# Performance work log

Measured on AMD Instinct MI355X. Metric: run time of the kernel, lower is better.

## Reference

```python
import jax, jax.numpy as jnp
import numpy as np

N_SUBWORDS = 8192
N_WORDS = 6000
HIDDEN = 1024


def setup_inputs() -> dict:
    key = jax.random.key(0)
    k_h, k_s, k_w = jax.random.split(key, 3)
    hidden_states = jax.random.normal(k_h, (N_SUBWORDS, HIDDEN), dtype=jnp.float32)
    # sorted start indices of words; ends are inclusive and contiguous up to the next start
    word_starts = jnp.sort(jax.random.randint(k_s, (N_WORDS,), 0, N_SUBWORDS, dtype=jnp.int64))
    nxt = jnp.concatenate([word_starts[1:], jnp.array([N_SUBWORDS], dtype=jnp.int64)])
    word_ends = jnp.maximum(nxt - 1, word_starts)  # inclusive ends, >= starts
    # params of self.subword_attn = Linear(hidden_size, 1)
    w_attn = jax.random.normal(k_w, (HIDDEN, 1), dtype=jnp.float32) * 0.02
    b_attn = jnp.zeros((1,), dtype=jnp.float32)
    return {
        "hidden_states": hidden_states,
        "word_starts": word_starts,
        "word_ends": word_ends,
        "w_attn": w_attn,
        "b_attn": b_attn,
    }


def reference(hidden_states, word_starts, word_ends, w_attn, b_attn):
    """Word-encoder masked attention pooling (wl-coref _wordencoder_attn_scores + pooling).

    hidden_states: [n_subwords, hidden]
    word_starts/word_ends: [n_words] inclusive span boundaries over subwords
    Returns pooled word embeddings: [n_words, hidden]
    """
    n_sub = hidden_states.shape[0]
    pos = jnp.arange(n_sub)  # [n_subwords]
    # torch: (arange >= starts) * (arange < ends+1)  -> inclusive end mask
    mask = (pos[None, :] >= word_starts[:, None]) & (pos[None, :] <= word_ends[:, None])
    # per-subword scalar score: Linear(hidden, 1), broadcast to [n_words, n_subwords]
    scores = (hidden_states @ w_attn + b_attn).T  # [1, n_subwords]
    # torch adds log(mask.float()) == -inf outside span; scores are finite
    logits = jnp.where(mask, scores, -jnp.inf)
    attn = jax.nn.softmax(logits, axis=1)  # [n_words, n_subwords]
    # pool subword embeddings into word embeddings
    return attn @ hidden_states  # [n_words, hidden]
```

## Files before the change

### kernel.cpp

```cpp
#include <hip/hip_runtime.h>
#include <hip/hip_bf16.h>
#include <math.h>

#define N_SUBWORDS 8192
#define N_WORDS    6000
#define HIDDEN     1024

__global__ __launch_bounds__(256) void coref_fused_wave_kernel(
    const float* __restrict__ hs,
    const int*   __restrict__ starts,
    const int*   __restrict__ ends,
    const float* __restrict__ w_attn,
    const float* __restrict__ b_attn,
    float*       __restrict__ out)
{
    const int tid  = threadIdx.x;
    const int lane = tid & 63;
    const int w    = blockIdx.x * 4 + (tid >> 6);
    if (w >= N_WORDS) return;

    const int s0 = starts[w];
    const int s1 = ends[w];

    const float4* __restrict__ wvp = (const float4*)w_attn;
    float4 wv[4];
#pragma unroll
    for (int j = 0; j < 4; ++j)
        wv[j] = wvp[lane + 64 * j];
    const float b = b_attn[0];

    float  m = 0.f, l = 1.f;
    float4 acc[4];

    for (int s = s0; s <= s1; ++s) {
        const float4* __restrict__ row = (const float4*)(hs + (size_t)s * HIDDEN);
        float4 h[4];
#pragma unroll
        for (int j = 0; j < 4; ++j)
            h[j] = row[lane + 64 * j];

        float part = 0.f;
#pragma unroll
        for (int j = 0; j < 4; ++j)
            part += h[j].x * wv[j].x + h[j].y * wv[j].y +
                    h[j].z * wv[j].z + h[j].w * wv[j].w;

#pragma unroll
        for (int off = 32; off > 0; off >>= 1)
            part += __shfl_xor(part, off, 64);

        const float score = part + b;

        if (s == s0) {
            m = score;
            l = 1.f;
#pragma unroll
            for (int j = 0; j < 4; ++j)
                acc[j] = h[j];
        } else {
            const float mn    = fmaxf(m, score);
            const float alpha = __expf(m - mn);
            const float p     = __expf(score - mn);
            m = mn;
            l = l * alpha + p;
#pragma unroll
            for (int j = 0; j < 4; ++j) {
                acc[j].x = acc[j].x * alpha + p * h[j].x;
                acc[j].y = acc[j].y * alpha + p * h[j].y;
                acc[j].z = acc[j].z * alpha + p * h[j].z;
                acc[j].w = acc[j].w * alpha + p * h[j].w;
            }
        }
    }

    const float inv_l = 1.f / l;
    float4* __restrict__ orow = (float4*)(out + (size_t)w * HIDDEN);
#pragma unroll
    for (int j = 0; j < 4; ++j) {
        float4 o;
        o.x = acc[j].x * inv_l;
        o.y = acc[j].y * inv_l;
        o.z = acc[j].z * inv_l;
        o.w = acc[j].w * inv_l;
        orow[lane + 64 * j] = o;
    }
}

extern "C" void kernel_launch(void* const* d_in, const int* in_sizes, int n_in,
                              void* d_out, int out_size, void* d_ws, size_t ws_size,
                              hipStream_t stream) {
    const float* hs     = (const float*)d_in[0];
    const int*   starts = (const int*)d_in[1];
    const int*   ends   = (const int*)d_in[2];
    const float* w_attn = (const float*)d_in[3];
    const float* b_attn = (const float*)d_in[4];
    float*       out    = (float*)d_out;

    coref_fused_wave_kernel<<<dim3((N_WORDS + 3) / 4), dim3(256), 0, stream>>>(
        hs, starts, ends, w_attn, b_attn, out);
}
```

Before: 90.86 us.

## Split score computation into separate kernel and use two-pass softmax pooling

```diff
diff --git a/kernel.cpp b/kernel.cpp
--- a/kernel.cpp
+++ b/kernel.cpp
@@ -1,17 +1,45 @@
 #include <hip/hip_runtime.h>
-#include <hip/hip_bf16.h>
 #include <math.h>
 
 #define N_SUBWORDS 8192
 #define N_WORDS    6000
 #define HIDDEN     1024
 
-__global__ __launch_bounds__(256) void coref_fused_wave_kernel(
+__global__ __launch_bounds__(256) void coref_score_kernel(
+    const float* __restrict__ hs,
+    const float* __restrict__ w_attn,
+    const float* __restrict__ b_attn,
+    float*       __restrict__ scores)
+{
+    const int tid  = threadIdx.x;
+    const int lane = tid & 63;
+    const int row  = blockIdx.x * 4 + (tid >> 6);
+    if (row >= N_SUBWORDS) return;
+
+    const float4* __restrict__ wvp = (const float4*)w_attn;
+    const float4* __restrict__ rp  = (const float4*)(hs + (size_t)row * HIDDEN);
+
+    float part = 0.f;
+#pragma unroll
+    for (int j = 0; j < 4; ++j) {
+        const float4 h  = rp[lane + 64 * j];
+        const float4 wv = wvp[lane + 64 * j];
+        part += h.x * wv.x + h.y * wv.y + h.z * wv.z + h.w * wv.w;
+    }
+
+#pragma unroll
+    for (int off = 32; off > 0; off >>= 1)
+        part += __shfl_xor(part, off, 64);
+
+    if (lane == 0)
+        scores[row] = part + b_attn[0];
+}
+
+__global__ __launch_bounds__(256) void coref_pool_kernel(
     const float* __restrict__ hs,
     const int*   __restrict__ starts,
     const int*   __restrict__ ends,
-    const float* __restrict__ w_attn,
-    const float* __restrict__ b_attn,
+    const float* __restrict__ scores,
     float*       __restrict__ out)
 {
     const int tid  = threadIdx.x;
@@ -22,54 +50,27 @@
     const int s0 = starts[w];
     const int s1 = ends[w];
 
-    const float4* __restrict__ wvp = (const float4*)w_attn;
-    float4 wv[4];
+    float m = -INFINITY;
+    for (int s = s0; s <= s1; ++s)
+        m = fmaxf(m, scores[s]);
+
+    float  l = 0.f;
+    float4 acc[4];
 #pragma unroll
     for (int j = 0; j < 4; ++j)
-        wv[j] = wvp[lane + 64 * j];
-    const float b = b_attn[0];
-
-    float  m = 0.f, l = 1.f;
-    float4 acc[4];
+        acc[j] = make_float4(0.f, 0.f, 0.f, 0.f);
 
     for (int s = s0; s <= s1; ++s) {
+        const float p = __expf(scores[s] - m);
+        l += p;
         const float4* __restrict__ row = (const float4*)(hs + (size_t)s * HIDDEN);
-        float4 h[4];
 #pragma unroll
-        for (int j = 0; j < 4; ++j)
-            h[j] = row[lane + 64 * j];
-
-        float part = 0.f;
-#pragma unroll
-        for (int j = 0; j < 4; ++j)
-            part += h[j].x * wv[j].x + h[j].y * wv[j].y +
-                    h[j].z * wv[j].z + h[j].w * wv[j].w;
-
-#pragma unroll
-        for (int off = 32; off > 0; off >>= 1)
-            part += __shfl_xor(part, off, 64);
-
-        const float score = part + b;
-
-        if (s == s0) {
-            m = score;
-            l = 1.f;
-#pragma unroll
-            for (int j = 0; j < 4; ++j)
-                acc[j] = h[j];
-        } else {
-            const float mn    = fmaxf(m, score);
-            const float alpha = __expf(m - mn);
-            const float p     = __expf(score - mn);
-            m = mn;
-            l = l * alpha + p;
-#pragma unroll
-            for (int j = 0; j < 4; ++j) {
-                acc[j].x = acc[j].x * alpha + p * h[j].x;
-                acc[j].y = acc[j].y * alpha + p * h[j].y;
-                acc[j].z = acc[j].z * alpha + p * h[j].z;
-                acc[j].w = acc[j].w * alpha + p * h[j].w;
-            }
+        for (int j = 0; j < 4; ++j) {
+            const float4 h = row[lane + 64 * j];
+            acc[j].x += p * h.x;
+            acc[j].y += p * h.y;
+            acc[j].z += p * h.z;
+            acc[j].w += p * h.w;
         }
     }
 
@@ -95,7 +96,11 @@
     const float* w_attn = (const float*)d_in[3];
     const float* b_attn = (const float*)d_in[4];
     float*       out    = (float*)d_out;
+    float*       scores = (float*)d_ws;
 
-    coref_fused_wave_kernel<<<dim3((N_WORDS + 3) / 4), dim3(256), 0, stream>>>(
-        hs, starts, ends, w_attn, b_attn, out);
+    coref_score_kernel<<<dim3(N_SUBWORDS / 4), dim3(256), 0, stream>>>(
+        hs, w_attn, b_attn, scores);
+
+    coref_pool_kernel<<<dim3((N_WORDS + 3) / 4), dim3(256), 0, stream>>>(
+        hs, starts, ends, scores, out);
 }
```

Measured after the change: 96.32 us. 6.0% more time.

## Process four subword rows per online-softmax step and fast-path single-subword words

Applied to the files above, without the earlier changes.

```diff
diff --git a/kernel.cpp b/kernel.cpp
--- a/kernel.cpp
+++ b/kernel.cpp
@@ -1,12 +1,11 @@
 #include <hip/hip_runtime.h>
-#include <hip/hip_bf16.h>
 #include <math.h>
 
 #define N_SUBWORDS 8192
 #define N_WORDS    6000
 #define HIDDEN     1024
 
-__global__ __launch_bounds__(256) void coref_fused_wave_kernel(
+__global__ __launch_bounds__(256) void coref_fused_kernel(
     const float* __restrict__ hs,
     const int*   __restrict__ starts,
     const int*   __restrict__ ends,
@@ -16,11 +15,22 @@
 {
     const int tid  = threadIdx.x;
     const int lane = tid & 63;
-    const int w    = blockIdx.x * 4 + (tid >> 6);
+    const int w = __builtin_amdgcn_readfirstlane(blockIdx.x * 4 + (tid >> 6));
     if (w >= N_WORDS) return;
 
     const int s0 = starts[w];
     const int s1 = ends[w];
+
+    const float4* __restrict__ hs4  = (const float4*)hs;
+    float4*       __restrict__ orow = (float4*)(out + (size_t)w * HIDDEN);
+
+    if (s1 <= s0) {
+        const float4* __restrict__ row = hs4 + (size_t)s0 * (HIDDEN / 4);
+#pragma unroll
+        for (int j = 0; j < 4; ++j)
+            orow[lane + 64 * j] = row[lane + 64 * j];
+        return;
+    }
 
     const float4* __restrict__ wvp = (const float4*)w_attn;
     float4 wv[4];
@@ -29,52 +39,75 @@
         wv[j] = wvp[lane + 64 * j];
     const float b = b_attn[0];
 
-    float  m = 0.f, l = 1.f;
+    float  m = -INFINITY, l = 0.f;
     float4 acc[4];
+#pragma unroll
+    for (int j = 0; j < 4; ++j)
+        acc[j] = make_float4(0.f, 0.f, 0.f, 0.f);
 
-    for (int s = s0; s <= s1; ++s) {
-        const float4* __restrict__ row = (const float4*)(hs + (size_t)s * HIDDEN);
-        float4 h[4];
+    for (int s = s0; s <= s1; s += 4) {
+        const int C = (s1 - s + 1 < 4) ? (s1 - s + 1) : 4;
+
+        float4 h[4][4];
+        float  part[4];
 #pragma unroll
-        for (int j = 0; j < 4; ++j)
-            h[j] = row[lane + 64 * j];
-
-        float part = 0.f;
+        for (int c = 0; c < 4; ++c) {
+            part[c] = 0.f;
+            if (c < C) {
+                const float4* __restrict__ row =
+                    hs4 + (size_t)(s + c) * (HIDDEN / 4);
 #pragma unroll
-        for (int j = 0; j < 4; ++j)
-            part += h[j].x * wv[j].x + h[j].y * wv[j].y +
-                    h[j].z * wv[j].z + h[j].w * wv[j].w;
+                for (int j = 0; j < 4; ++j) {
+                    h[c][j] = row[lane + 64 * j];
+                    part[c] += h[c][j].x * wv[j].x + h[c][j].y * wv[j].y +
+                               h[c][j].z * wv[j].z + h[c][j].w * wv[j].w;
+                }
+            }
+        }
 
 #pragma unroll
-        for (int off = 32; off > 0; off >>= 1)
-            part += __shfl_xor(part, off, 64);
+        for (int off = 32; off > 0; off >>= 1) {
+#pragma unroll
+            for (int c = 0; c < 4; ++c)
+                part[c] += __shfl_xor(part[c], off, 64);
+        }
 
-        const float score = part + b;
+        float cm = -INFINITY;
+#pragma unroll
+        for (int c = 0; c < 4; ++c)
+            if (c < C) cm = fmaxf(cm, part[c] + b);
 
-        if (s == s0) {
-            m = score;
-            l = 1.f;
+        const float mn    = fmaxf(m, cm);
+        const float alpha = __expf(m - mn);
+        l *= alpha;
 #pragma unroll
-            for (int j = 0; j < 4; ++j)
-                acc[j] = h[j];
-        } else {
-            const float mn    = fmaxf(m, score);
-            const float alpha = __expf(m - mn);
-            const float p     = __expf(score - mn);
-            m = mn;
-            l = l * alpha + p;
+        for (int j = 0; j < 4; ++j) {
+            acc[j].x *= alpha; acc[j].y *= alpha;
+            acc[j].z *= alpha; acc[j].w *= alpha;
+        }
+
+        float p[4];
 #pragma unroll
-            for (int j = 0; j < 4; ++j) {
-                acc[j].x = acc[j].x * alpha + p * h[j].x;
-                acc[j].y = acc[j].y * alpha + p * h[j].y;
-                acc[j].z = acc[j].z * alpha + p * h[j].z;
-                acc[j].w = acc[j].w * alpha + p * h[j].w;
+        for (int c = 0; c < 4; ++c) {
+            p[c] = (c < C) ? __expf(part[c] + b - mn) : 0.f;
+            l += p[c];
+        }
+#pragma unroll
+        for (int c = 0; c < 4; ++c) {
+            if (c < C) {
+#pragma unroll
+                for (int j = 0; j < 4; ++j) {
+                    acc[j].x += p[c] * h[c][j].x;
+                    acc[j].y += p[c] * h[c][j].y;
+                    acc[j].z += p[c] * h[c][j].z;
+                    acc[j].w += p[c] * h[c][j].w;
+                }
             }
         }
+        m = mn;
     }
 
     const float inv_l = 1.f / l;
-    float4* __restrict__ orow = (float4*)(out + (size_t)w * HIDDEN);
 #pragma unroll
     for (int j = 0; j < 4; ++j) {
         float4 o;
@@ -96,6 +129,6 @@
     const float* b_attn = (const float*)d_in[4];
     float*       out    = (float*)d_out;
 
-    coref_fused_wave_kernel<<<dim3((N_WORDS + 3) / 4), dim3(256), 0, stream>>>(
+    coref_fused_kernel<<<dim3((N_WORDS + 3) / 4), dim3(256), 0, stream>>>(
         hs, starts, ends, w_attn, b_attn, out);
 }
```

After: 89.64 us. Within noise of the previous version (-1.3%).
